# Kernel optimization log

Hardware: AMD Instinct MI355X
Metric: run time of the kernel (lower is better)

## Reference

```python
import itertools
import jax, jax.numpy as jnp
import numpy as np


def setup_inputs() -> dict:
    key = jax.random.key(0)
    k1, k2 = jax.random.split(key)
    B, X, Y, Z, C = 2, 160, 192, 160, 1
    vol = jax.random.normal(k1, (B, X, Y, Z, C), dtype=jnp.float32)
    trf = jax.random.normal(k2, (B, X, Y, Z, 3), dtype=jnp.float32)  # dense displacement field
    return {"vol": vol, "trf": trf}


def _warp(vol, trf):
    # vol: [B, *spatial, C]; trf: [B, *spatial, nd] displacement (indexing='ij')
    B = vol.shape[0]
    spatial = vol.shape[1:-1]
    nd = len(spatial)
    C = vol.shape[-1]
    N = int(np.prod(spatial))

    grids = jnp.meshgrid(*[jnp.arange(s, dtype=jnp.float32) for s in spatial], indexing="ij")
    # absolute sample locations per dim: [B, *spatial]
    loc = [grids[d][None] + trf[..., d] for d in range(nd)]

    max_loc = [s - 1 for s in spatial]
    loc0 = [jnp.clip(jnp.floor(loc[d]), 0.0, max_loc[d]) for d in range(nd)]
    loc1 = [jnp.clip(loc0[d] + 1.0, 0.0, max_loc[d]) for d in range(nd)]
    clipped = [jnp.clip(loc[d], 0.0, max_loc[d]) for d in range(nd)]
    # neurite weight convention: weight for corner bit 0 is (loc1 - loc), for bit 1 is (1 - that)
    w1 = [loc1[d] - clipped[d] for d in range(nd)]   # weight when corner uses loc0
    w0 = [1.0 - w1[d] for d in range(nd)]            # weight when corner uses loc1
    i0 = [loc0[d].astype(jnp.int32) for d in range(nd)]
    i1 = [loc1[d].astype(jnp.int32) for d in range(nd)]

    vol_flat = vol.reshape(B, N, C)

    out = jnp.zeros((B,) + spatial + (C,), dtype=vol.dtype)
    for corner in itertools.product([0, 1], repeat=nd):
        subs = [(i1[d] if corner[d] else i0[d]) for d in range(nd)]
        ind = subs[0]
        for d in range(1, nd):
            ind = ind * spatial[d] + subs[d]  # row-major sub2ind
        vals = jnp.take_along_axis(vol_flat, ind.reshape(B, N)[..., None], axis=1)
        vals = vals.reshape((B,) + spatial + (C,))
        wt = (w0[0] if corner[0] else w1[0])
        for d in range(1, nd):
            wt = wt * (w0[d] if corner[d] else w1[d])
        out = out + wt[..., None] * vals
    return out


def reference(vol, trf):
    # indexing='ij', single_transform=False, fill_value=None (clamp to edge), linear interp.
    # The layer also passes trf through unchanged; we return the warped volume.
    return _warp(vol, trf)
```

## Files before the change

kernel.cpp:

```cpp
#include <hip/hip_runtime.h>

constexpr int B = 2, X = 160, Y = 192, Z = 160;
constexpr int TXs = 8, TYs = 8, TZs = 16;
constexpr int XT = X / TXs, YT = Y / TYs, ZT = Z / TZs;
constexpr int NTILES = B * XT * YT * ZT;
constexpr int NXCD = 8;
constexpr int CHUNK = NTILES / NXCD;
constexpr int RX = 16, RY = 16, RZ = 32;
constexpr int NROWS = RX * RY;
constexpr int RSTRIDE = RZ + 1;
constexpr int LDSF = NROWS * RSTRIDE;

typedef float f32x4 __attribute__((ext_vector_type(4)));
typedef float f32x2a __attribute__((ext_vector_type(2), aligned(4)));

__global__ __launch_bounds__(256) void warp_kernel(
    const float* __restrict__ vol,
    const float* __restrict__ trf,
    float* __restrict__ out)
{
    __shared__ float lds[LDSF];

    const int tid = threadIdx.x;
    const int bid = blockIdx.x;

    const int eff = (bid & (NXCD - 1)) * CHUNK + (bid >> 3);

    int tz = eff % ZT;
    int r  = eff / ZT;
    int ty = r % YT;
    int r2 = r / YT;
    int tx = r2 % XT;
    int b  = r2 / XT;

    const int xs = tx * TXs - 4;
    const int ys = ty * TYs - 4;
    const int zs = tz * TZs - 8;

#pragma unroll
    for (int k = 0; k < 8; ++k) {
        int c   = tid + k * 256;
        int row = c >> 3;
        int j   = c & 7;
        int xi  = row >> 4;
        int yi  = row & 15;
        int xg  = min(max(xs + xi, 0), X - 1);
        int yg  = min(max(ys + yi, 0), Y - 1);
        int zg  = min(max(zs + 4 * j, 0), Z - 4);
        const f32x4 v = *reinterpret_cast<const f32x4*>(
            vol + ((size_t)(b * X + xg) * Y + yg) * Z + zg);
        int a = row * RSTRIDE + 4 * j;
        lds[a + 0] = v.x;
        lds[a + 1] = v.y;
        lds[a + 2] = v.z;
        lds[a + 3] = v.w;
    }
    __syncthreads();

    int zq = tid & 3;
    int ly = (tid >> 2) & 7;
    int lx = tid >> 5;
    int x  = tx * TXs + lx;
    int y  = ty * TYs + ly;
    int z0v = tz * TZs + 4 * zq;

    size_t vid0 = ((size_t)(b * X + x) * Y + y) * Z + z0v;

    const f32x4* tp = reinterpret_cast<const f32x4*>(trf + vid0 * 3);
    f32x4 t0 = tp[0], t1 = tp[1], t2 = tp[2];
    float d[12] = {t0.x, t0.y, t0.z, t0.w,
                   t1.x, t1.y, t1.z, t1.w,
                   t2.x, t2.y, t2.z, t2.w};

    const float mx = (float)(X - 1), my = (float)(Y - 1), mz = (float)(Z - 1);
    const float fx = (float)x, fy = (float)y;
    const int bX = b * X;

    float res[4];
#pragma unroll
    for (int e = 0; e < 4; ++e) {
        float lxf = fx + d[3 * e + 0];
        float lyf = fy + d[3 * e + 1];
        float lzf = (float)(z0v + e) + d[3 * e + 2];

        float lx0 = fminf(fmaxf(floorf(lxf), 0.0f), mx);
        float lx1 = fminf(lx0 + 1.0f, mx);
        float clx = fminf(fmaxf(lxf, 0.0f), mx);
        float wxA = lx1 - clx, wxB = 1.0f - wxA;
        int ix0 = (int)lx0, ix1 = (int)lx1;

        float ly0 = fminf(fmaxf(floorf(lyf), 0.0f), my);
        float ly1 = fminf(ly0 + 1.0f, my);
        float cly = fminf(fmaxf(lyf, 0.0f), my);
        float wyA = ly1 - cly, wyB = 1.0f - wyA;
        int iy0 = (int)ly0, iy1 = (int)ly1;

        float lz0 = fminf(fmaxf(floorf(lzf), 0.0f), mz);
        float lz1 = fminf(lz0 + 1.0f, mz);
        float clz = fminf(fmaxf(lzf, 0.0f), mz);
        float wzA = lz1 - clz, wzB = 1.0f - wzA;
        int iz0 = (int)lz0, iz1 = (int)lz1;

        int ux0 = ix0 - xs, ux1 = ix1 - xs;
        int uy0 = iy0 - ys, uy1 = iy1 - ys;
        int uz0 = iz0 - zs, uz1 = iz1 - zs;

        bool ok = ((unsigned)ux0 < (unsigned)RX) & ((unsigned)ux1 < (unsigned)RX) &
                  ((unsigned)uy0 < (unsigned)RY) & ((unsigned)uy1 < (unsigned)RY) &
                  ((unsigned)uz0 < (unsigned)RZ) & ((unsigned)uz1 < (unsigned)RZ);

        float v000, v001, v010, v011, v100, v101, v110, v111;
        if (ok) {
            bool edge = (iz1 == iz0);
            int r00 = ((ux0 << 4) + uy0) * RSTRIDE + uz0;
            int r01 = ((ux0 << 4) + uy1) * RSTRIDE + uz0;
            int r10 = ((ux1 << 4) + uy0) * RSTRIDE + uz0;
            int r11 = ((ux1 << 4) + uy1) * RSTRIDE + uz0;
            f32x2a p00 = *reinterpret_cast<const f32x2a*>(&lds[r00]);
            f32x2a p01 = *reinterpret_cast<const f32x2a*>(&lds[r01]);
            f32x2a p10 = *reinterpret_cast<const f32x2a*>(&lds[r10]);
            f32x2a p11 = *reinterpret_cast<const f32x2a*>(&lds[r11]);
            v000 = p00.x; v001 = edge ? p00.x : p00.y;
            v010 = p01.x; v011 = edge ? p01.x : p01.y;
            v100 = p10.x; v101 = edge ? p10.x : p10.y;
            v110 = p11.x; v111 = edge ? p11.x : p11.y;
        } else {
            size_t g00 = ((size_t)(bX + ix0) * Y + iy0) * Z;
            size_t g01 = ((size_t)(bX + ix0) * Y + iy1) * Z;
            size_t g10 = ((size_t)(bX + ix1) * Y + iy0) * Z;
            size_t g11 = ((size_t)(bX + ix1) * Y + iy1) * Z;
            v000 = vol[g00 + iz0];
            v001 = vol[g00 + iz1];
            v010 = vol[g01 + iz0];
            v011 = vol[g01 + iz1];
            v100 = vol[g10 + iz0];
            v101 = vol[g10 + iz1];
            v110 = vol[g11 + iz0];
            v111 = vol[g11 + iz1];
        }

        res[e] = wxA * (wyA * (wzA * v000 + wzB * v001) +
                        wyB * (wzA * v010 + wzB * v011)) +
                 wxB * (wyA * (wzA * v100 + wzB * v101) +
                        wyB * (wzA * v110 + wzB * v111));
    }

    f32x4 o;
    o.x = res[0]; o.y = res[1]; o.z = res[2]; o.w = res[3];
    *reinterpret_cast<f32x4*>(out + vid0) = o;
}

extern "C" void kernel_launch(void* const* d_in, const int* in_sizes, int n_in,
                              void* d_out, int out_size, void* d_ws, size_t ws_size,
                              hipStream_t stream) {
    const float* vol = (const float*)d_in[0];
    const float* trf = (const float*)d_in[1];
    float* out = (float*)d_out;

    warp_kernel<<<NTILES, 256, 0, stream>>>(vol, trf, out);
}
```

Before: 41.58 us.

## Shrink LDS halo in z and simplify corner addressing and edge handling

Reduces the z extent of the shared-memory halo tile from 32 to 24, so each block stages 6 float4 loads per thread instead of 8 and uses less LDS. A launch_bounds hint asks for 6 resident blocks per CU. Corner addresses are now derived from one base offset plus deltas, and the z-edge case is folded into the weights rather than handled with per-value selects. The smaller halo means more samples with large z displacement miss the tile and take the slower global-memory path.

```diff
diff --git a/kernel.cpp b/kernel.cpp
--- a/kernel.cpp
+++ b/kernel.cpp
@@ -6,7 +6,7 @@
 constexpr int NTILES = B * XT * YT * ZT;
 constexpr int NXCD = 8;
 constexpr int CHUNK = NTILES / NXCD;
-constexpr int RX = 16, RY = 16, RZ = 32;
+constexpr int RX = 16, RY = 16, RZ = 24;
 constexpr int NROWS = RX * RY;
 constexpr int RSTRIDE = RZ + 1;
 constexpr int LDSF = NROWS * RSTRIDE;
@@ -14,7 +14,7 @@
 typedef float f32x4 __attribute__((ext_vector_type(4)));
 typedef float f32x2a __attribute__((ext_vector_type(2), aligned(4)));
 
-__global__ __launch_bounds__(256) void warp_kernel(
+__global__ __launch_bounds__(256, 6) void warp_kernel(
     const float* __restrict__ vol,
     const float* __restrict__ trf,
     float* __restrict__ out)
@@ -35,25 +35,30 @@
 
     const int xs = tx * TXs - 4;
     const int ys = ty * TYs - 4;
-    const int zs = tz * TZs - 8;
+    const int zs = tz * TZs - 4;
 
+    {
+        int row = (tid * 171) >> 10;
+        int j   = tid - 6 * row;
 #pragma unroll
-    for (int k = 0; k < 8; ++k) {
-        int c   = tid + k * 256;
-        int row = c >> 3;
-        int j   = c & 7;
-        int xi  = row >> 4;
-        int yi  = row & 15;
-        int xg  = min(max(xs + xi, 0), X - 1);
-        int yg  = min(max(ys + yi, 0), Y - 1);
-        int zg  = min(max(zs + 4 * j, 0), Z - 4);
-        const f32x4 v = *reinterpret_cast<const f32x4*>(
-            vol + ((size_t)(b * X + xg) * Y + yg) * Z + zg);
-        int a = row * RSTRIDE + 4 * j;
-        lds[a + 0] = v.x;
-        lds[a + 1] = v.y;
-        lds[a + 2] = v.z;
-        lds[a + 3] = v.w;
+        for (int k = 0; k < 6; ++k) {
+            int xi = row >> 4;
+            int yi = row & 15;
+            int xg = min(max(xs + xi, 0), X - 1);
+            int yg = min(max(ys + yi, 0), Y - 1);
+            int zg = min(max(zs + 4 * j, 0), Z - 4);
+            const f32x4 v = *reinterpret_cast<const f32x4*>(
+                vol + ((size_t)(b * X + xg) * Y + yg) * Z + zg);
+            int a = row * RSTRIDE + 4 * j;
+            lds[a + 0] = v.x;
+            lds[a + 1] = v.y;
+            lds[a + 2] = v.z;
+            lds[a + 3] = v.w;
+            int jn = j + 4;
+            bool wrap = (jn >= 6);
+            j   = wrap ? jn - 6 : jn;
+            row += wrap ? 43 : 42;
+        }
     }
     __syncthreads();
 
@@ -101,29 +106,34 @@
         float wzA = lz1 - clz, wzB = 1.0f - wzA;
         int iz0 = (int)lz0, iz1 = (int)lz1;
 
+        bool edge = (iz1 == iz0);
+        float wzAe = edge ? 1.0f : wzA;
+        float wzBe = edge ? 0.0f : wzB;
+
         int ux0 = ix0 - xs, ux1 = ix1 - xs;
         int uy0 = iy0 - ys, uy1 = iy1 - ys;
-        int uz0 = iz0 - zs, uz1 = iz1 - zs;
+        int uz0 = iz0 - zs;
 
         bool ok = ((unsigned)ux0 < (unsigned)RX) & ((unsigned)ux1 < (unsigned)RX) &
                   ((unsigned)uy0 < (unsigned)RY) & ((unsigned)uy1 < (unsigned)RY) &
-                  ((unsigned)uz0 < (unsigned)RZ) & ((unsigned)uz1 < (unsigned)RZ);
+                  ((unsigned)uz0 < (unsigned)(RZ - 1));
 
         float v000, v001, v010, v011, v100, v101, v110, v111;
         if (ok) {
-            bool edge = (iz1 == iz0);
+            int dY  = (iy1 > iy0) ? RSTRIDE : 0;
+            int dXx = (ix1 > ix0) ? (RSTRIDE * 16) : 0;
             int r00 = ((ux0 << 4) + uy0) * RSTRIDE + uz0;
-            int r01 = ((ux0 << 4) + uy1) * RSTRIDE + uz0;
-            int r10 = ((ux1 << 4) + uy0) * RSTRIDE + uz0;
-            int r11 = ((ux1 << 4) + uy1) * RSTRIDE + uz0;
+            int r01 = r00 + dY;
+            int r10 = r00 + dXx;
+            int r11 = r10 + dY;
             f32x2a p00 = *reinterpret_cast<const f32x2a*>(&lds[r00]);
             f32x2a p01 = *reinterpret_cast<const f32x2a*>(&lds[r01]);
             f32x2a p10 = *reinterpret_cast<const f32x2a*>(&lds[r10]);
             f32x2a p11 = *reinterpret_cast<const f32x2a*>(&lds[r11]);
-            v000 = p00.x; v001 = edge ? p00.x : p00.y;
-            v010 = p01.x; v011 = edge ? p01.x : p01.y;
-            v100 = p10.x; v101 = edge ? p10.x : p10.y;
-            v110 = p11.x; v111 = edge ? p11.x : p11.y;
+            v000 = p00.x; v001 = p00.y;
+            v010 = p01.x; v011 = p01.y;
+            v100 = p10.x; v101 = p10.y;
+            v110 = p11.x; v111 = p11.y;
         } else {
             size_t g00 = ((size_t)(bX + ix0) * Y + iy0) * Z;
             size_t g01 = ((size_t)(bX + ix0) * Y + iy1) * Z;
@@ -139,10 +149,10 @@
             v111 = vol[g11 + iz1];
         }
 
-        res[e] = wxA * (wyA * (wzA * v000 + wzB * v001) +
-                        wyB * (wzA * v010 + wzB * v011)) +
-                 wxB * (wyA * (wzA * v100 + wzB * v101) +
-                        wyB * (wzA * v110 + wzB * v111));
+        res[e] = wxA * (wyA * (wzAe * v000 + wzBe * v001) +
+                        wyB * (wzAe * v010 + wzBe * v011)) +
+                 wxB * (wyA * (wzAe * v100 + wzBe * v101) +
+                        wyB * (wzAe * v110 + wzBe * v111));
     }
 
     f32x4 o;
```

New measurement: 40.40 us. 2.8% less time.
